# Optimization experiments

Measured on AMD Instinct MI355X. Metric: run time of the kernel, lower is better.

The kernel has to match this reference:

```python
import jax, jax.numpy as jnp
import numpy as np

SEQ, BATCH, IN = 512, 64, 1024
H, L = 512, 2


def setup_inputs() -> dict:
    key = jax.random.key(0)
    ks = jax.random.split(key, 5)
    s = 0.02
    return {
        "x": jax.random.normal(ks[0], (SEQ, BATCH, IN), dtype=jnp.float32),
        "W_ih": jax.random.normal(ks[1], (L, 2, 4 * H, IN), dtype=jnp.float32) * s,
        "b_ih": jax.random.normal(ks[2], (L, 2, 4 * H), dtype=jnp.float32) * s,
        "W_hh": jax.random.normal(ks[3], (L, 2, 4 * H, H), dtype=jnp.float32) * s,
        "b_hh": jax.random.normal(ks[4], (L, 2, 4 * H), dtype=jnp.float32) * s,
    }


def _run_direction(xs, Wi, bi, Wh, bh, hidden):
    # Precompute the input projection for all timesteps in one big GEMM.
    pre = jnp.einsum("tbd,gd->tbg", xs, Wi) + bi  # [T, B, 4H]

    def step(carry, p):
        h, c = carry
        gates = p + h @ Wh.T + bh
        i, f, g, o = jnp.split(gates, 4, axis=-1)
        # NOTE: faithful to the source module's (nonstandard) gating:
        #   c_t = c_{t-1} * sigmoid(i) + sigmoid(f) * tanh(g)
        c = c * jax.nn.sigmoid(i) + jax.nn.sigmoid(f) * jnp.tanh(g)
        h = jnp.tanh(c) * jax.nn.sigmoid(o)
        return (h, c), h

    B = xs.shape[1]
    h0 = jnp.zeros((B, hidden), xs.dtype)
    c0 = jnp.zeros((B, hidden), xs.dtype)
    _, hs = jax.lax.scan(step, (h0, c0), pre)
    return hs  # [T, B, H]


def reference(x, W_ih, b_ih, W_hh, b_hh):
    hidden = W_hh.shape[-1]
    num_layers = W_ih.shape[0]
    inp = x  # [T, B, D]
    for l in range(num_layers):
        fwd = _run_direction(inp, W_ih[l, 0], b_ih[l, 0], W_hh[l, 0], b_hh[l, 0], hidden)
        bwd = _run_direction(inp[::-1], W_ih[l, 1], b_ih[l, 1], W_hh[l, 1], b_hh[l, 1], hidden)[::-1]
        inp = jnp.concatenate([fwd, bwd], axis=-1)  # [T, B, 2H]
    return inp
```

## Files before the change

kernel.cpp:

```cpp
#include <hip/hip_runtime.h>

#define TSEQ 512
#define BATCH 64
#define DIN 1024
#define HID 512
#define G4 2048
#define CHK 64

typedef __attribute__((ext_vector_type(8))) short short8;
typedef __attribute__((ext_vector_type(4))) float floatx4;

__device__ __forceinline__ floatx4 mfma16(short8 a, short8 b, floatx4 c) {
  return __builtin_amdgcn_mfma_f32_16x16x32_bf16(a, b, c, 0, 0, 0);
}

__device__ __forceinline__ unsigned short f2bf(float f) {
  unsigned int u = __float_as_uint(f);
  unsigned int r = (u + 0x7fffu + ((u >> 16) & 1u)) >> 16;
  return (unsigned short)r;
}

__device__ __forceinline__ float sigm(float x) { return 1.f / (1.f + __expf(-x)); }
__device__ __forceinline__ float tanh_f(float x) {
  float xx = fminf(fmaxf(x, -15.f), 15.f);
  float e = __expf(2.f * xx);
  return (e - 1.f) / (e + 1.f);
}

__device__ __forceinline__ unsigned long long coh_load_q(const unsigned long long* p) {
  return __hip_atomic_load(p, __ATOMIC_RELAXED, __HIP_MEMORY_SCOPE_AGENT);
}
__device__ __forceinline__ unsigned int coh_load_u32(const unsigned int* p) {
  return __hip_atomic_load(p, __ATOMIC_RELAXED, __HIP_MEMORY_SCOPE_AGENT);
}
__device__ __forceinline__ void coh_store_u32(unsigned int* p, unsigned int v) {
  __hip_atomic_store(p, v, __ATOMIC_RELAXED, __HIP_MEMORY_SCOPE_AGENT);
}

__global__ void k_convert_x(const float* __restrict__ x, unsigned short* __restrict__ xbf, int n4) {
  int i = blockIdx.x * 256 + threadIdx.x;
  if (i >= n4) return;
  floatx4 v = reinterpret_cast<const floatx4*>(x)[i];
  union { unsigned short us[4]; unsigned long long ull; } pk;
  pk.us[0] = f2bf(v[0]); pk.us[1] = f2bf(v[1]); pk.us[2] = f2bf(v[2]); pk.us[3] = f2bf(v[3]);
  reinterpret_cast<unsigned long long*>(xbf)[i] = pk.ull;
}

__global__ void k_prep_w(const float* __restrict__ W, unsigned short* __restrict__ Wf, int K) {
  int mt = blockIdx.x, kt = blockIdx.y, ld = blockIdx.z;
  int lane = threadIdx.x;
  int i = lane & 15;
  int unit = (mt >> 1) * 8 + (i >> 2) * 2 + (mt & 1);
  int row = (i & 3) * HID + unit;
  int k0 = kt * 32 + (lane >> 4) * 8;
  const float* src = W + (size_t)ld * G4 * K + (size_t)row * K + k0;
  unsigned short* dst = Wf + (size_t)ld * G4 * K + (((size_t)mt * (K / 32) + kt) * 64 + lane) * 8;
  for (int j = 0; j < 8; ++j) dst[j] = f2bf(src[j]);
}

__global__ void k_prep_bias(const float* __restrict__ bih, const float* __restrict__ bhh,
                            float* __restrict__ biasf) {
  int idx = blockIdx.x * 256 + threadIdx.x;
  int ld = idx >> 11;
  int rp = idx & 2047;
  int unit = (rp >> 5) * 8 + ((rp >> 2) & 3) * 2 + ((rp >> 4) & 1);
  int row = (rp & 3) * HID + unit;
  biasf[idx] = bih[ld * G4 + row] + bhh[ld * G4 + row];
}

__global__ void k_zero_bar(unsigned int* bar) {
  int i = threadIdx.x;
  if (i < 128) bar[i * 16] = 0;
}

__global__ __launch_bounds__(256, 2) void k_proj(
    const unsigned short* __restrict__ xin,
    const unsigned short* __restrict__ Wf,
    const float* __restrict__ biasf,
    float* __restrict__ pre,
    int t0) {
  const int dir = blockIdx.z;
  const int w = threadIdx.x >> 6;
  const int lane = threadIdx.x & 63;
  const int quad = lane >> 4, col = lane & 15;
  const int tloc = blockIdx.y * 4 + w;
  const int tg = dir ? (TSEQ - 1 - (t0 + tloc)) : (t0 + tloc);
  const unsigned short* Wd = Wf + (size_t)dir * G4 * DIN;
  const unsigned short* xrow = xin + (size_t)tg * BATCH * DIN;

  floatx4 acc[8][4];
#pragma unroll
  for (int mi = 0; mi < 8; ++mi)
#pragma unroll
    for (int ni = 0; ni < 4; ++ni) acc[mi][ni] = (floatx4){0.f, 0.f, 0.f, 0.f};

#pragma unroll 4
  for (int kt = 0; kt < 32; ++kt) {
    short8 bfr[4];
#pragma unroll
    for (int ni = 0; ni < 4; ++ni) {
      int b = ni * 16 + col;
      bfr[ni] = *reinterpret_cast<const short8*>(xrow + (size_t)b * DIN + kt * 32 + quad * 8);
    }
#pragma unroll
    for (int mi = 0; mi < 8; ++mi) {
      size_t mt = (size_t)(blockIdx.x * 8 + mi);
      short8 afr = *reinterpret_cast<const short8*>(Wd + ((mt * 32 + kt) * 64 + lane) * 8);
#pragma unroll
      for (int ni = 0; ni < 4; ++ni) acc[mi][ni] = mfma16(afr, bfr[ni], acc[mi][ni]);
    }
  }

#pragma unroll
  for (int mi = 0; mi < 8; ++mi) {
    int gbase = blockIdx.x * 128 + mi * 16 + quad * 4;
#pragma unroll
    for (int r = 0; r < 4; ++r) {
      float bv = biasf[dir * G4 + gbase + r];
      float* prow = pre + (((size_t)dir * CHK + tloc) * G4 + gbase + r) * BATCH;
#pragma unroll
      for (int ni = 0; ni < 4; ++ni) prow[ni * 16 + col] = acc[mi][ni][r] + bv;
    }
  }
}

__device__ __forceinline__ void wait_flags(const unsigned int* flags, unsigned int target) {
  const int lane = threadIdx.x & 63;
  const unsigned int* p = flags + lane * 16;
  while (true) {
    unsigned int v = coh_load_u32(p);
    if (__all((int)(v >= target))) break;
    __builtin_amdgcn_s_sleep(1);
  }
}

__global__ __launch_bounds__(256, 1) void k_steps(
    const unsigned short* __restrict__ Whhf,
    const float* __restrict__ pre,
    unsigned short* act1bf,
    unsigned short* hT2,
    float* cst,
    float* __restrict__ dout,
    unsigned int* bar,
    int t0, int layer, unsigned int bar_base) {
  const int dir = blockIdx.y;
  const int gb = blockIdx.x;
  const int w = threadIdx.x >> 6;
  const int lane = threadIdx.x & 63;
  const int quad = lane >> 4, col = lane & 15;
  const int b = w * 16 + col;
  unsigned int* flags = bar + dir * 1024;

  __shared__ unsigned short wlds[32 * HID];
  {
    const uint4* src = reinterpret_cast<const uint4*>(
        Whhf + (size_t)dir * G4 * HID + (size_t)gb * 16384);
    uint4* dst = reinterpret_cast<uint4*>(wlds);
#pragma unroll
    for (int it = 0; it < 8; ++it) dst[it * 256 + threadIdx.x] = src[it * 256 + threadIdx.x];
  }

  float* cl = cst + ((size_t)layer * 2 + dir) * HID * BATCH;
  const int u0 = gb * 8 + quad * 2;
  const int u1 = u0 + 1;
  float c0 = 0.f, c1 = 0.f;
  if (t0 > 0) { c0 = cl[u0 * BATCH + b]; c1 = cl[u1 * BATCH + b]; }

  float pf[2][4];
#pragma unroll
  for (int mi = 0; mi < 2; ++mi)
#pragma unroll
    for (int r = 0; r < 4; ++r) {
      int gp = gb * 32 + mi * 16 + quad * 4 + r;
      pf[mi][r] = pre[(((size_t)dir * CHK + 0) * G4 + gp) * BATCH + b];
    }

  __syncthreads();

  for (int j = 0; j < CHK; ++j) {
    const int s = t0 + j;
    const int t = dir ? (TSEQ - 1 - s) : s;

    floatx4 acc[2];
#pragma unroll
    for (int mi = 0; mi < 2; ++mi)
#pragma unroll
      for (int r = 0; r < 4; ++r) acc[mi][r] = pf[mi][r];

    if (j + 1 < CHK) {
#pragma unroll
      for (int mi = 0; mi < 2; ++mi)
#pragma unroll
        for (int r = 0; r < 4; ++r) {
          int gp = gb * 32 + mi * 16 + quad * 4 + r;
          pf[mi][r] = pre[(((size_t)dir * CHK + (j + 1)) * G4 + gp) * BATCH + b];
        }
    }

    if (s > 0) {
      if (j >= 1) wait_flags(flags, bar_base + (unsigned)j);

      const unsigned short* hprev;
      int hstride;
      if (layer == 0) {
        int tp = dir ? t + 1 : t - 1;
        hprev = act1bf + (size_t)tp * BATCH * DIN + dir * HID;
        hstride = DIN;
      } else {
        hprev = hT2 + (size_t)(((s - 1) & 1) * 2 + dir) * BATCH * HID;
        hstride = HID;
      }
      const unsigned long long* hq =
          reinterpret_cast<const unsigned long long*>(hprev + (size_t)b * hstride);
      short8 hb[16];
#pragma unroll
      for (int kt = 0; kt < 16; ++kt) {
        union { unsigned long long q[2]; short8 v; } u;
        u.q[0] = coh_load_q(hq + kt * 8 + quad * 2);
        u.q[1] = coh_load_q(hq + kt * 8 + quad * 2 + 1);
        hb[kt] = u.v;
      }
#pragma unroll
      for (int kt = 0; kt < 16; ++kt) {
        short8 w0 = *reinterpret_cast<const short8*>(wlds + ((0 * 16 + kt) * 64 + lane) * 8);
        short8 w1 = *reinterpret_cast<const short8*>(wlds + ((1 * 16 + kt) * 64 + lane) * 8);
        acc[0] = mfma16(w0, hb[kt], acc[0]);
        acc[1] = mfma16(w1, hb[kt], acc[1]);
      }
    }

    float si = sigm(acc[0][0]);
    float sf = sigm(acc[0][1]);
    float tg = tanh_f(acc[0][2]);
    float so = sigm(acc[0][3]);
    c0 = c0 * si + sf * tg;
    float h0 = tanh_f(c0) * so;

    si = sigm(acc[1][0]);
    sf = sigm(acc[1][1]);
    tg = tanh_f(acc[1][2]);
    so = sigm(acc[1][3]);
    c1 = c1 * si + sf * tg;
    float h1 = tanh_f(c1) * so;

    unsigned int hp = (unsigned int)f2bf(h0) | ((unsigned int)f2bf(h1) << 16);
    if (layer == 0) {
      unsigned short* arow = act1bf + ((size_t)t * BATCH + b) * DIN + dir * HID;
      coh_store_u32(reinterpret_cast<unsigned int*>(arow + u0), hp);
    } else {
      unsigned short* hrow2 = hT2 + ((size_t)((s & 1) * 2 + dir) * BATCH + b) * HID;
      coh_store_u32(reinterpret_cast<unsigned int*>(hrow2 + u0), hp);
      float* drow = dout + ((size_t)t * BATCH + b) * DIN + dir * HID;
      *reinterpret_cast<float2*>(drow + u0) = make_float2(h0, h1);
    }

    if (j + 1 < CHK) {
      __syncthreads();
      if (threadIdx.x == 0) coh_store_u32(flags + gb * 16, bar_base + (unsigned)(j + 1));
    }
  }

  cl[u0 * BATCH + b] = c0;
  cl[u1 * BATCH + b] = c1;
}

extern "C" void kernel_launch(void* const* d_in, const int* in_sizes, int n_in,
                              void* d_out, int out_size, void* d_ws, size_t ws_size,
                              hipStream_t stream) {
  const float* x = (const float*)d_in[0];
  const float* W_ih = (const float*)d_in[1];
  const float* b_ih = (const float*)d_in[2];
  const float* W_hh = (const float*)d_in[3];
  const float* b_hh = (const float*)d_in[4];
  float* dout = (float*)d_out;

  char* p = (char*)d_ws;
  auto alloc = [&](size_t bytes) {
    char* r = p;
    p += (bytes + 255) & ~(size_t)255;
    return r;
  };
  unsigned short* xbf    = (unsigned short*)alloc((size_t)TSEQ * BATCH * DIN * 2);
  unsigned short* act1bf = (unsigned short*)alloc((size_t)TSEQ * BATCH * DIN * 2);
  float*          pre    = (float*)alloc((size_t)2 * CHK * G4 * BATCH * 4);
  unsigned short* Wihf   = (unsigned short*)alloc((size_t)4 * G4 * DIN * 2);
  unsigned short* Whhf   = (unsigned short*)alloc((size_t)4 * G4 * HID * 2);
  float*          biasf  = (float*)alloc((size_t)4 * G4 * 4);
  float*          cst    = (float*)alloc((size_t)4 * HID * BATCH * 4);
  unsigned short* hT2    = (unsigned short*)alloc((size_t)4 * BATCH * HID * 2);
  unsigned int*   bar    = (unsigned int*)alloc((size_t)2 * 64 * 16 * 4);

  size_t required = (size_t)(p - (char*)d_ws);
  if (ws_size < required) return;

  int n4 = TSEQ * BATCH * DIN / 4;
  k_zero_bar<<<dim3(1), dim3(128), 0, stream>>>(bar);
  k_convert_x<<<dim3((n4 + 255) / 256), dim3(256), 0, stream>>>(x, xbf, n4);
  k_prep_w<<<dim3(G4 / 16, DIN / 32, 4), dim3(64), 0, stream>>>(W_ih, Wihf, DIN);
  k_prep_w<<<dim3(G4 / 16, HID / 32, 4), dim3(64), 0, stream>>>(W_hh, Whhf, HID);
  k_prep_bias<<<dim3(32), dim3(256), 0, stream>>>(b_ih, b_hh, biasf);

  unsigned int bar_base = 0;
  for (int l = 0; l < 2; ++l) {
    const unsigned short* xin = l ? act1bf : xbf;
    const unsigned short* Wfl = Wihf + (size_t)l * 2 * G4 * DIN;
    const unsigned short* Whl = Whhf + (size_t)l * 2 * G4 * HID;
    const float* bfl = biasf + (size_t)l * 2 * G4;
    for (int c = 0; c < TSEQ / CHK; ++c) {
      k_proj<<<dim3(G4 / 128, CHK / 4, 2), dim3(256), 0, stream>>>(xin, Wfl, bfl, pre, c * CHK);
      k_steps<<<dim3(G4 / 32, 2), dim3(256), 0, stream>>>(Whl, pre, act1bf, hT2, cst, dout,
                                                          bar, c * CHK, l, bar_base);
      bar_base += (unsigned)(CHK - 1);
    }
  }
  (void)in_sizes; (void)n_in; (void)out_size;
}
```

Measured before the change: 6.490 ms.

## Merge both directions into one block grid with per-wave flag sync

The recurrent kernel now runs 64 blocks, each handling both directions in an interleaved loop, with both directions' W_hh slices held in LDS. The block-wide __syncthreads before each flag publish is replaced by per-wave flags published after a vmcnt wait, and waiters poll 256 flags through four loads per lane. The prefetch of next-step preactivations moves after the flag store. The aim is to hide one direction's sync latency behind the other's work and drop the intra-block barrier. The cost is double the LDS per block, half as many blocks, and more flag polling traffic.

```diff
diff --git a/kernel.cpp b/kernel.cpp
--- a/kernel.cpp
+++ b/kernel.cpp
@@ -6,6 +6,7 @@
 #define HID 512
 #define G4 2048
 #define CHK 64
+#define NBLK 64
 
 typedef __attribute__((ext_vector_type(8))) short short8;
 typedef __attribute__((ext_vector_type(4))) float floatx4;
@@ -69,8 +70,8 @@
 }
 
 __global__ void k_zero_bar(unsigned int* bar) {
-  int i = threadIdx.x;
-  if (i < 128) bar[i * 16] = 0;
+  int i = blockIdx.x * 256 + threadIdx.x;
+  if (i < 512) bar[i * 16] = 0;
 }
 
 __global__ __launch_bounds__(256, 2) void k_proj(
@@ -124,12 +125,16 @@
   }
 }
 
-__device__ __forceinline__ void wait_flags(const unsigned int* flags, unsigned int target) {
+__device__ __forceinline__ void wait_chain(const unsigned int* flags, unsigned int target) {
   const int lane = threadIdx.x & 63;
   const unsigned int* p = flags + lane * 16;
   while (true) {
-    unsigned int v = coh_load_u32(p);
-    if (__all((int)(v >= target))) break;
+    unsigned int v0 = coh_load_u32(p);
+    unsigned int v1 = coh_load_u32(p + 64 * 16);
+    unsigned int v2 = coh_load_u32(p + 128 * 16);
+    unsigned int v3 = coh_load_u32(p + 192 * 16);
+    unsigned int mn = min(min(v0, v1), min(v2, v3));
+    if (__all((int)(mn >= target))) break;
     __builtin_amdgcn_s_sleep(1);
   }
 }
@@ -143,125 +148,138 @@
     float* __restrict__ dout,
     unsigned int* bar,
     int t0, int layer, unsigned int bar_base) {
-  const int dir = blockIdx.y;
   const int gb = blockIdx.x;
   const int w = threadIdx.x >> 6;
   const int lane = threadIdx.x & 63;
   const int quad = lane >> 4, col = lane & 15;
   const int b = w * 16 + col;
-  unsigned int* flags = bar + dir * 1024;
-
-  __shared__ unsigned short wlds[32 * HID];
-  {
+
+  __shared__ unsigned short wlds[2][32 * HID];
+#pragma unroll
+  for (int d = 0; d < 2; ++d) {
     const uint4* src = reinterpret_cast<const uint4*>(
-        Whhf + (size_t)dir * G4 * HID + (size_t)gb * 16384);
-    uint4* dst = reinterpret_cast<uint4*>(wlds);
+        Whhf + (size_t)d * G4 * HID + (size_t)gb * 16384);
+    uint4* dst = reinterpret_cast<uint4*>(wlds[d]);
 #pragma unroll
     for (int it = 0; it < 8; ++it) dst[it * 256 + threadIdx.x] = src[it * 256 + threadIdx.x];
   }
 
-  float* cl = cst + ((size_t)layer * 2 + dir) * HID * BATCH;
   const int u0 = gb * 8 + quad * 2;
   const int u1 = u0 + 1;
-  float c0 = 0.f, c1 = 0.f;
-  if (t0 > 0) { c0 = cl[u0 * BATCH + b]; c1 = cl[u1 * BATCH + b]; }
-
-  float pf[2][4];
-#pragma unroll
-  for (int mi = 0; mi < 2; ++mi)
-#pragma unroll
-    for (int r = 0; r < 4; ++r) {
-      int gp = gb * 32 + mi * 16 + quad * 4 + r;
-      pf[mi][r] = pre[(((size_t)dir * CHK + 0) * G4 + gp) * BATCH + b];
-    }
+  float c0[2] = {0.f, 0.f}, c1[2] = {0.f, 0.f};
+  if (t0 > 0) {
+#pragma unroll
+    for (int d = 0; d < 2; ++d) {
+      const float* cl = cst + ((size_t)layer * 2 + d) * HID * BATCH;
+      c0[d] = cl[u0 * BATCH + b];
+      c1[d] = cl[u1 * BATCH + b];
+    }
+  }
+
+  float pf[2][2][4];
+#pragma unroll
+  for (int d = 0; d < 2; ++d)
+#pragma unroll
+    for (int mi = 0; mi < 2; ++mi)
+#pragma unroll
+      for (int r = 0; r < 4; ++r) {
+        int gp = gb * 32 + mi * 16 + quad * 4 + r;
+        pf[d][mi][r] = pre[(((size_t)d * CHK + 0) * G4 + gp) * BATCH + b];
+      }
 
   __syncthreads();
 
+#pragma unroll 1
   for (int j = 0; j < CHK; ++j) {
     const int s = t0 + j;
-    const int t = dir ? (TSEQ - 1 - s) : s;
-
-    floatx4 acc[2];
-#pragma unroll
-    for (int mi = 0; mi < 2; ++mi)
-#pragma unroll
-      for (int r = 0; r < 4; ++r) acc[mi][r] = pf[mi][r];
-
-    if (j + 1 < CHK) {
+#pragma unroll
+    for (int d = 0; d < 2; ++d) {
+      const int t = d ? (TSEQ - 1 - s) : s;
+      unsigned int* flags_d = bar + d * 256 * 16;
+
+      floatx4 acc[2];
 #pragma unroll
       for (int mi = 0; mi < 2; ++mi)
 #pragma unroll
-        for (int r = 0; r < 4; ++r) {
-          int gp = gb * 32 + mi * 16 + quad * 4 + r;
-          pf[mi][r] = pre[(((size_t)dir * CHK + (j + 1)) * G4 + gp) * BATCH + b];
+        for (int r = 0; r < 4; ++r) acc[mi][r] = pf[d][mi][r];
+
+      if (s > 0) {
+        if (j >= 1) wait_chain(flags_d, bar_base + (unsigned)j);
+
+        const unsigned short* hprev;
+        int hstride;
+        if (layer == 0) {
+          int tp = d ? t + 1 : t - 1;
+          hprev = act1bf + (size_t)tp * BATCH * DIN + d * HID;
+          hstride = DIN;
+        } else {
+          hprev = hT2 + (size_t)(((s - 1) & 1) * 2 + d) * BATCH * HID;
+          hstride = HID;
         }
-    }
-
-    if (s > 0) {
-      if (j >= 1) wait_flags(flags, bar_base + (unsigned)j);
-
-      const unsigned short* hprev;
-      int hstride;
+        const unsigned long long* hq =
+            reinterpret_cast<const unsigned long long*>(hprev + (size_t)b * hstride);
+        short8 hb[16];
+#pragma unroll
+        for (int kt = 0; kt < 16; ++kt) {
+          union { unsigned long long q[2]; short8 v; } u;
+          u.q[0] = coh_load_q(hq + kt * 8 + quad * 2);
+          u.q[1] = coh_load_q(hq + kt * 8 + quad * 2 + 1);
+          hb[kt] = u.v;
+        }
+#pragma unroll
+        for (int kt = 0; kt < 16; ++kt) {
+          short8 w0 = *reinterpret_cast<const short8*>(wlds[d] + ((0 * 16 + kt) * 64 + lane) * 8);
+          short8 w1 = *reinterpret_cast<const short8*>(wlds[d] + ((1 * 16 + kt) * 64 + lane) * 8);
+          acc[0] = mfma16(w0, hb[kt], acc[0]);
+          acc[1] = mfma16(w1, hb[kt], acc[1]);
+        }
+      }
+
+      float si = sigm(acc[0][0]);
+      float sf = sigm(acc[0][1]);
+      float tg = tanh_f(acc[0][2]);
+      float so = sigm(acc[0][3]);
+      c0[d] = c0[d] * si + sf * tg;
+      float h0 = tanh_f(c0[d]) * so;
+
+      si = sigm(acc[1][0]);
+      sf = sigm(acc[1][1]);
+      tg = tanh_f(acc[1][2]);
+      so = sigm(acc[1][3]);
+      c1[d] = c1[d] * si + sf * tg;
+      float h1 = tanh_f(c1[d]) * so;
+
+      unsigned int hp = (unsigned int)f2bf(h0) | ((unsigned int)f2bf(h1) << 16);
       if (layer == 0) {
-        int tp = dir ? t + 1 : t - 1;
-        hprev = act1bf + (size_t)tp * BATCH * DIN + dir * HID;
-        hstride = DIN;
+        unsigned short* arow = act1bf + ((size_t)t * BATCH + b) * DIN + d * HID;
+        coh_store_u32(reinterpret_cast<unsigned int*>(arow + u0), hp);
       } else {
-        hprev = hT2 + (size_t)(((s - 1) & 1) * 2 + dir) * BATCH * HID;
-        hstride = HID;
+        unsigned short* hrow2 = hT2 + ((size_t)((s & 1) * 2 + d) * BATCH + b) * HID;
+        coh_store_u32(reinterpret_cast<unsigned int*>(hrow2 + u0), hp);
+        float* drow = dout + ((size_t)t * BATCH + b) * DIN + d * HID;
+        *reinterpret_cast<float2*>(drow + u0) = make_float2(h0, h1);
       }
-      const unsigned long long* hq =
-          reinterpret_cast<const unsigned long long*>(hprev + (size_t)b * hstride);
-      short8 hb[16];
-#pragma unroll
-      for (int kt = 0; kt < 16; ++kt) {
-        union { unsigned long long q[2]; short8 v; } u;
-        u.q[0] = coh_load_q(hq + kt * 8 + quad * 2);
-        u.q[1] = coh_load_q(hq + kt * 8 + quad * 2 + 1);
-        hb[kt] = u.v;
+
+      if (j + 1 < CHK) {
+        asm volatile("s_waitcnt vmcnt(0)" ::: "memory");
+        if (lane == 0) coh_store_u32(flags_d + (gb * 4 + w) * 16, bar_base + (unsigned)(j + 1));
+#pragma unroll
+        for (int mi = 0; mi < 2; ++mi)
+#pragma unroll
+          for (int r = 0; r < 4; ++r) {
+            int gp = gb * 32 + mi * 16 + quad * 4 + r;
+            pf[d][mi][r] = pre[(((size_t)d * CHK + (j + 1)) * G4 + gp) * BATCH + b];
+          }
       }
-#pragma unroll
-      for (int kt = 0; kt < 16; ++kt) {
-        short8 w0 = *reinterpret_cast<const short8*>(wlds + ((0 * 16 + kt) * 64 + lane) * 8);
-        short8 w1 = *reinterpret_cast<const short8*>(wlds + ((1 * 16 + kt) * 64 + lane) * 8);
-        acc[0] = mfma16(w0, hb[kt], acc[0]);
-        acc[1] = mfma16(w1, hb[kt], acc[1]);
-      }
-    }
-
-    float si = sigm(acc[0][0]);
-    float sf = sigm(acc[0][1]);
-    float tg = tanh_f(acc[0][2]);
-    float so = sigm(acc[0][3]);
-    c0 = c0 * si + sf * tg;
-    float h0 = tanh_f(c0) * so;
-
-    si = sigm(acc[1][0]);
-    sf = sigm(acc[1][1]);
-    tg = tanh_f(acc[1][2]);
-    so = sigm(acc[1][3]);
-    c1 = c1 * si + sf * tg;
-    float h1 = tanh_f(c1) * so;
-
-    unsigned int hp = (unsigned int)f2bf(h0) | ((unsigned int)f2bf(h1) << 16);
-    if (layer == 0) {
-      unsigned short* arow = act1bf + ((size_t)t * BATCH + b) * DIN + dir * HID;
-      coh_store_u32(reinterpret_cast<unsigned int*>(arow + u0), hp);
-    } else {
-      unsigned short* hrow2 = hT2 + ((size_t)((s & 1) * 2 + dir) * BATCH + b) * HID;
-      coh_store_u32(reinterpret_cast<unsigned int*>(hrow2 + u0), hp);
-      float* drow = dout + ((size_t)t * BATCH + b) * DIN + dir * HID;
-      *reinterpret_cast<float2*>(drow + u0) = make_float2(h0, h1);
-    }
-
-    if (j + 1 < CHK) {
-      __syncthreads();
-      if (threadIdx.x == 0) coh_store_u32(flags + gb * 16, bar_base + (unsigned)(j + 1));
-    }
-  }
-
-  cl[u0 * BATCH + b] = c0;
-  cl[u1 * BATCH + b] = c1;
+    }
+  }
+
+#pragma unroll
+  for (int d = 0; d < 2; ++d) {
+    float* cl = cst + ((size_t)layer * 2 + d) * HID * BATCH;
+    cl[u0 * BATCH + b] = c0[d];
+    cl[u1 * BATCH + b] = c1[d];
+  }
 }
 
 extern "C" void kernel_launch(void* const* d_in, const int* in_sizes, int n_in,
@@ -288,13 +306,13 @@
   float*          biasf  = (float*)alloc((size_t)4 * G4 * 4);
   float*          cst    = (float*)alloc((size_t)4 * HID * BATCH * 4);
   unsigned short* hT2    = (unsigned short*)alloc((size_t)4 * BATCH * HID * 2);
-  unsigned int*   bar    = (unsigned int*)alloc((size_t)2 * 64 * 16 * 4);
+  unsigned int*   bar    = (unsigned int*)alloc((size_t)2 * 256 * 16 * 4);
 
   size_t required = (size_t)(p - (char*)d_ws);
   if (ws_size < required) return;
 
   int n4 = TSEQ * BATCH * DIN / 4;
-  k_zero_bar<<<dim3(1), dim3(128), 0, stream>>>(bar);
+  k_zero_bar<<<dim3(2), dim3(256), 0, stream>>>(bar);
   k_convert_x<<<dim3((n4 + 255) / 256), dim3(256), 0, stream>>>(x, xbf, n4);
   k_prep_w<<<dim3(G4 / 16, DIN / 32, 4), dim3(64), 0, stream>>>(W_ih, Wihf, DIN);
   k_prep_w<<<dim3(G4 / 16, HID / 32, 4), dim3(64), 0, stream>>>(W_hh, Whhf, HID);
@@ -308,8 +326,8 @@
     const float* bfl = biasf + (size_t)l * 2 * G4;
     for (int c = 0; c < TSEQ / CHK; ++c) {
       k_proj<<<dim3(G4 / 128, CHK / 4, 2), dim3(256), 0, stream>>>(xin, Wfl, bfl, pre, c * CHK);
-      k_steps<<<dim3(G4 / 32, 2), dim3(256), 0, stream>>>(Whl, pre, act1bf, hT2, cst, dout,
-                                                          bar, c * CHK, l, bar_base);
+      k_steps<<<dim3(NBLK), dim3(256), 0, stream>>>(Whl, pre, act1bf, hT2, cst, dout,
+                                                    bar, c * CHK, l, bar_base);
       bar_base += (unsigned)(CHK - 1);
     }
   }
```

New measurement: 11.45 ms. 1.76x slower.
